# Kernel tuning notes

Hardware: AMD Instinct MI355X
Metric: run time of the kernel (lower is better)

The kernel has to match this reference:

```python
import jax, jax.numpy as jnp
import numpy as np

N = 524288
H = 128

def _mlp(x, w1, b1, w2, b2, w3, b3):
    # torch nn.Linear: y = x @ W^T + b, weights stored (out,in)
    x = jax.nn.relu(x @ w1.T + b1)
    x = jax.nn.relu(x @ w2.T + b2)
    return x @ w3.T + b3

def _det2(F):
    return F[:, 0, 0] * F[:, 1, 1] - F[:, 0, 1] * F[:, 1, 0]

def setup_inputs() -> dict:
    key = jax.random.key(0)
    ks = jax.random.split(key, 13)
    def lin(k, out_d, in_d):
        s = 1.0 / np.sqrt(in_d)
        kw, kb = jax.random.split(k)
        return (jax.random.uniform(kw, (out_d, in_d), jnp.float32, -s, s),
                jax.random.uniform(kb, (out_d,), jnp.float32, -s, s))
    F = jax.random.normal(ks[0], (N, 2, 2), jnp.float32)
    dc_w1, dc_b1 = lin(ks[1], H, 7)
    dc_w2, dc_b2 = lin(ks[2], H, H)
    dc_w3, dc_b3 = lin(ks[3], 4, H)
    sp_w1, sp_b1 = lin(ks[4], H, 3)
    sp_w2, sp_b2 = lin(ks[5], H, H)
    sp_w3, sp_b3 = lin(ks[6], 4, H)
    return dict(F=F, dc_w1=dc_w1, dc_b1=dc_b1, dc_w2=dc_w2, dc_b2=dc_b2,
                dc_w3=dc_w3, dc_b3=dc_b3, sp_w1=sp_w1, sp_b1=sp_b1,
                sp_w2=sp_w2, sp_b2=sp_b2, sp_w3=sp_w3, sp_b3=sp_b3)

def reference(F, dc_w1, dc_b1, dc_w2, dc_b2, dc_w3, dc_b3,
              sp_w1, sp_b1, sp_w2, sp_b2, sp_w3, sp_b3):
    I = jnp.eye(2, dtype=F.dtype)
    F = F.reshape(-1, 2, 2)
    # --- DeformationCorrector ---
    U, sig, Vh = jnp.linalg.svd(F)
    R = U @ Vh
    FtF = jnp.einsum('nji,njk->nik', F, F)  # F^T F
    I1 = sig - 1.0                           # (N,2)
    I2 = (FtF - I).reshape(-1, 4)            # (N,4)
    I3 = _det2(F)[:, None] - 1.0             # (N,1)
    inv = jnp.concatenate([I1, I2, I3], axis=1)  # (N,7)
    x = _mlp(inv, dc_w1, dc_b1, dc_w2, dc_b2, dc_w3, dc_b3).reshape(-1, 2, 2)
    x = (x + jnp.swapaxes(x, 1, 2)) * 0.5
    Fp = R @ x + F
    # --- StressPredictorFromFp ---
    U2, sig2, Vh2 = jnp.linalg.svd(Fp)
    R2 = U2 @ Vh2
    J1 = sig2.sum(axis=1) - 2.0
    J2 = jnp.sum(Fp * Fp, axis=(1, 2)) - 1.0  # trace(Fp^T Fp) - 1
    J3 = _det2(Fp) - 1.0
    y = jnp.stack([J1, J2, J3], axis=1)       # (N,3)
    y = _mlp(y, sp_w1, sp_b1, sp_w2, sp_b2, sp_w3, sp_b3).reshape(-1, 2, 2)
    y = (y + jnp.swapaxes(y, 1, 2)) * 0.5
    P = R2 @ y
    cauchy = jnp.einsum('nij,nkj->nik', P, Fp)  # P @ Fp^T
    return cauchy.reshape(-1, 4)
```

## Files before the change

### kernel.cpp

```cpp
#include <hip/hip_runtime.h>

typedef float f32x4 __attribute__((ext_vector_type(4)));
typedef _Float16 f16x8 __attribute__((ext_vector_type(8)));

#define OFF_W2H 0
#define OFF_W2L 32768
#define OFF_W1  65536
#define OFF_W3H 73728
#define OFF_W3L 75008
#define OFF_B1  76288
#define OFF_B2  76800
#define OFF_B3  77312
#define LDS_BYTES 77328

__device__ inline float kdet(float a, float b, float c, float d) {
    float w = b * c;
    float e = fmaf(b, c, -w);
    return fmaf(a, d, -w) - e;
}

__device__ inline void polar2(float a, float b, float c, float d, float det,
                              float& R00, float& R01, float& R10, float& R11) {
    if (det >= 0.f) {
        float h1 = a + d, h2 = c - b;
        float q = fmaxf(sqrtf(h1 * h1 + h2 * h2), 1e-30f);
        float iq = 1.f / q;
        R00 = h1 * iq; R01 = -h2 * iq; R10 = h2 * iq; R11 = h1 * iq;
    } else {
        float h1 = a - d, h2 = b + c;
        float q = fmaxf(sqrtf(h1 * h1 + h2 * h2), 1e-30f);
        float iq = 1.f / q;
        R00 = h1 * iq; R01 = h2 * iq; R10 = h2 * iq; R11 = -h1 * iq;
    }
}

__device__ inline void stage_weights(unsigned char* s, const float* w1, int D,
                                     const float* b1, const float* w2, const float* b2,
                                     const float* w3, const float* b3) {
    const int tid = threadIdx.x, nt = blockDim.x;
    for (int idx = tid; idx < 2048; idx += nt) {
        int j = idx >> 4, kb = (idx >> 2) & 3, g = idx & 3;
        const float* src = w2 + j * 128 + kb * 32 + g * 4;
        f16x8 vh, vl;
        #pragma unroll
        for (int e = 0; e < 8; ++e) {
            float w = src[(e & 3) + 16 * (e >> 2)];
            _Float16 h = (_Float16)w;
            vh[e] = h;
            vl[e] = (_Float16)(w - (float)h);
        }
        int off = j * 256 + ((kb * 64 + g * 16) ^ ((j & 7) << 4));
        *(f16x8*)(s + OFF_W2H + off) = vh;
        *(f16x8*)(s + OFF_W2L + off) = vl;
    }
    for (int idx = tid; idx < 512; idx += nt) {
        int j = idx >> 2, g = idx & 3;
        f16x8 v;
        #pragma unroll
        for (int e = 0; e < 8; ++e) {
            int k = 4 * g + (e & 3) + 16 * (e >> 2);
            _Float16 val = (_Float16)0.f;
            if (k < D) val = (_Float16)w1[j * D + k];
            else if (k >= 8 && k < 8 + D) val = (_Float16)w1[j * D + (k - 8)];
            else if (k >= 16 && k < 16 + D) {
                float w = w1[j * D + (k - 16)];
                val = (_Float16)(w - (float)(_Float16)w);
            }
            v[e] = val;
        }
        int gg = g ^ ((j ^ (j >> 2)) & 3);
        *(f16x8*)(s + OFF_W1 + j * 64 + gg * 16) = v;
    }
    for (int idx = tid; idx < 80; idx += nt) {
        int j = idx >> 4, kb = (idx >> 2) & 3, g = idx & 3;
        f16x8 vh, vl;
        #pragma unroll
        for (int e = 0; e < 8; ++e) {
            int c = 32 * kb + 4 * g + (e & 3) + 16 * (e >> 2);
            float w = (j < 4) ? w3[j * 128 + c] : 0.f;
            _Float16 h = (_Float16)w;
            vh[e] = h;
            vl[e] = (_Float16)(w - (float)h);
        }
        int off = j * 256 + ((kb * 64 + g * 16) ^ ((j & 7) << 4));
        *(f16x8*)(s + OFF_W3H + off) = vh;
        *(f16x8*)(s + OFF_W3L + off) = vl;
    }
    for (int idx = tid; idx < 128; idx += nt) {
        ((float*)(s + OFF_B1))[idx] = b1[idx];
        ((float*)(s + OFF_B2))[idx] = b2[idx];
    }
    if (tid < 4) ((float*)(s + OFF_B3))[tid] = b3[tid];
}

__device__ inline f16x8 build_b1(const float* xin, int g) {
    _Float16 xh[8], xl[8];
    #pragma unroll
    for (int c = 0; c < 8; ++c) {
        float v = xin[c];
        _Float16 h = (_Float16)v;
        xh[c] = h;
        xl[c] = (_Float16)(v - (float)h);
    }
    const _Float16 z = (_Float16)0.f;
    f16x8 b;
    if (g == 0) {
        b[0] = xh[0]; b[1] = xh[1]; b[2] = xh[2]; b[3] = xh[3];
        b[4] = xh[0]; b[5] = xh[1]; b[6] = xh[2]; b[7] = xh[3];
    } else if (g == 1) {
        b[0] = xh[4]; b[1] = xh[5]; b[2] = xh[6]; b[3] = xh[7];
        b[4] = xh[4]; b[5] = xh[5]; b[6] = xh[6]; b[7] = xh[7];
    } else if (g == 2) {
        b[0] = xl[0]; b[1] = xl[1]; b[2] = xl[2]; b[3] = xl[3];
        b[4] = z; b[5] = z; b[6] = z; b[7] = z;
    } else {
        b[0] = xl[4]; b[1] = xl[5]; b[2] = xl[6]; b[3] = xl[7];
        b[4] = z; b[5] = z; b[6] = z; b[7] = z;
    }
    return b;
}

__device__ inline void mlp128(const unsigned char* s, f16x8 b1f, int m, int g,
                              float xout[4]) {
    const f32x4 zero = {0.f, 0.f, 0.f, 0.f};
    f32x4 acc[8];
    #pragma unroll
    for (int mb = 0; mb < 8; ++mb) {
        int row = m + 16 * mb;
        int gg = g ^ ((row ^ (row >> 2)) & 3);
        f16x8 af = *(const f16x8*)(s + OFF_W1 + row * 64 + gg * 16);
        acc[mb] = __builtin_amdgcn_mfma_f32_16x16x32_f16(af, b1f, zero, 0, 0, 0);
    }
    #pragma unroll
    for (int mb = 0; mb < 8; ++mb) {
        f32x4 bq = *(const f32x4*)(s + OFF_B1 + (mb * 16 + g * 4) * 4);
        #pragma unroll
        for (int r = 0; r < 4; ++r) acc[mb][r] = fmaxf(acc[mb][r] + bq[r], 0.f);
    }
    f16x8 hh[4], hl[4];
    #pragma unroll
    for (int kb = 0; kb < 4; ++kb)
        #pragma unroll
        for (int e = 0; e < 8; ++e) {
            float v = acc[2 * kb + (e >> 2)][e & 3];
            _Float16 h = (_Float16)v;
            hh[kb][e] = h;
            hl[kb][e] = (_Float16)(v - (float)h);
        }
    f32x4 acc2[8];
    #pragma unroll
    for (int mb = 0; mb < 8; ++mb) acc2[mb] = zero;
    #pragma unroll
    for (int mb = 0; mb < 8; ++mb) {
        int row = m + 16 * mb;
        #pragma unroll
        for (int kb = 0; kb < 4; ++kb) {
            int off = row * 256 + ((kb * 64 + g * 16) ^ ((row & 7) << 4));
            f16x8 ah = *(const f16x8*)(s + OFF_W2H + off);
            f16x8 al = *(const f16x8*)(s + OFF_W2L + off);
            acc2[mb] = __builtin_amdgcn_mfma_f32_16x16x32_f16(ah, hh[kb], acc2[mb], 0, 0, 0);
            acc2[mb] = __builtin_amdgcn_mfma_f32_16x16x32_f16(ah, hl[kb], acc2[mb], 0, 0, 0);
            acc2[mb] = __builtin_amdgcn_mfma_f32_16x16x32_f16(al, hh[kb], acc2[mb], 0, 0, 0);
        }
    }
    #pragma unroll
    for (int mb = 0; mb < 8; ++mb) {
        f32x4 bq = *(const f32x4*)(s + OFF_B2 + (mb * 16 + g * 4) * 4);
        #pragma unroll
        for (int r = 0; r < 4; ++r) acc2[mb][r] = fmaxf(acc2[mb][r] + bq[r], 0.f);
    }
    f16x8 h2h[4], h2l[4];
    #pragma unroll
    for (int kb = 0; kb < 4; ++kb)
        #pragma unroll
        for (int e = 0; e < 8; ++e) {
            float v = acc2[2 * kb + (e >> 2)][e & 3];
            _Float16 h = (_Float16)v;
            h2h[kb][e] = h;
            h2l[kb][e] = (_Float16)(v - (float)h);
        }
    f32x4 acc3 = zero;
    const int r3 = (m < 4) ? m : 4;
    #pragma unroll
    for (int kb = 0; kb < 4; ++kb) {
        int off = r3 * 256 + ((kb * 64 + g * 16) ^ ((r3 & 7) << 4));
        f16x8 ah = *(const f16x8*)(s + OFF_W3H + off);
        f16x8 al = *(const f16x8*)(s + OFF_W3L + off);
        acc3 = __builtin_amdgcn_mfma_f32_16x16x32_f16(ah, h2h[kb], acc3, 0, 0, 0);
        acc3 = __builtin_amdgcn_mfma_f32_16x16x32_f16(ah, h2l[kb], acc3, 0, 0, 0);
        acc3 = __builtin_amdgcn_mfma_f32_16x16x32_f16(al, h2h[kb], acc3, 0, 0, 0);
    }
    f32x4 b3q = *(const f32x4*)(s + OFF_B3);
    #pragma unroll
    for (int o = 0; o < 4; ++o)
        xout[o] = __shfl(acc3[o] + b3q[o], m, 64);
}

__global__ __launch_bounds__(512) void k_dc(const float* __restrict__ Fin,
    const float* __restrict__ w1, const float* __restrict__ b1,
    const float* __restrict__ w2, const float* __restrict__ b2,
    const float* __restrict__ w3, const float* __restrict__ b3,
    float* __restrict__ out, int nelem) {
    extern __shared__ unsigned char s[];
    stage_weights(s, w1, 7, b1, w2, b2, w3, b3);
    __syncthreads();
    const int lane = threadIdx.x & 63;
    const int m = lane & 15, g = lane >> 4;
    const int wid = blockIdx.x * (blockDim.x >> 6) + (threadIdx.x >> 6);
    const int nw = gridDim.x * (blockDim.x >> 6);
    const int niter = nelem >> 4;
    for (int it = wid; it < niter; it += nw) {
        const int elem = it * 16 + m;
        f32x4 f = ((const f32x4*)Fin)[elem];
        float a = f[0], b = f[1], c = f[2], d = f[3];
        float det = kdet(a, b, c, d);
        float R00, R01, R10, R11;
        polar2(a, b, c, d, det, R00, R01, R10, R11);
        float E = 0.5f * (a + d), Hh = 0.5f * (c - b);
        float Fv = 0.5f * (a - d), G = 0.5f * (b + c);
        float Q = sqrtf(E * E + Hh * Hh), Rr = sqrtf(Fv * Fv + G * G);
        float inv[8];
        inv[0] = Q + Rr - 1.f;
        inv[1] = fabsf(Q - Rr) - 1.f;
        inv[2] = fmaf(a, a, c * c) - 1.f;
        inv[3] = fmaf(a, b, c * d);
        inv[4] = inv[3];
        inv[5] = fmaf(b, b, d * d) - 1.f;
        inv[6] = det - 1.f;
        inv[7] = 0.f;
        f16x8 b1f = build_b1(inv, g);
        float x[4];
        mlp128(s, b1f, m, g, x);
        float x01 = 0.5f * (x[1] + x[2]);
        float Fp00 = fmaf(R00, x[0], fmaf(R01, x01, a));
        float Fp01 = fmaf(R00, x01, fmaf(R01, x[3], b));
        float Fp10 = fmaf(R10, x[0], fmaf(R11, x01, c));
        float Fp11 = fmaf(R10, x01, fmaf(R11, x[3], d));
        if (g == 0) {
            f32x4 r = {Fp00, Fp01, Fp10, Fp11};
            ((f32x4*)out)[elem] = r;
        }
    }
}

__global__ __launch_bounds__(512) void k_sp(float* io,
    const float* __restrict__ w1, const float* __restrict__ b1,
    const float* __restrict__ w2, const float* __restrict__ b2,
    const float* __restrict__ w3, const float* __restrict__ b3, int nelem) {
    extern __shared__ unsigned char s[];
    stage_weights(s, w1, 3, b1, w2, b2, w3, b3);
    __syncthreads();
    const int lane = threadIdx.x & 63;
    const int m = lane & 15, g = lane >> 4;
    const int wid = blockIdx.x * (blockDim.x >> 6) + (threadIdx.x >> 6);
    const int nw = gridDim.x * (blockDim.x >> 6);
    const int niter = nelem >> 4;
    for (int it = wid; it < niter; it += nw) {
        const int elem = it * 16 + m;
        f32x4 fp = ((const f32x4*)io)[elem];
        float a = fp[0], b = fp[1], c = fp[2], d = fp[3];
        float det = kdet(a, b, c, d);
        float R00, R01, R10, R11;
        polar2(a, b, c, d, det, R00, R01, R10, R11);
        float E = 0.5f * (a + d), Hh = 0.5f * (c - b);
        float Fv = 0.5f * (a - d), G = 0.5f * (b + c);
        float Q = sqrtf(E * E + Hh * Hh), Rr = sqrtf(Fv * Fv + G * G);
        float inv[8];
        inv[0] = (Q + Rr) + fabsf(Q - Rr) - 2.f;
        inv[1] = fmaf(a, a, fmaf(b, b, fmaf(c, c, d * d))) - 1.f;
        inv[2] = det - 1.f;
        inv[3] = 0.f; inv[4] = 0.f; inv[5] = 0.f; inv[6] = 0.f; inv[7] = 0.f;
        f16x8 b1f = build_b1(inv, g);
        float y[4];
        mlp128(s, b1f, m, g, y);
        float y01 = 0.5f * (y[1] + y[2]);
        float P00 = fmaf(R00, y[0], R01 * y01);
        float P01 = fmaf(R00, y01, R01 * y[3]);
        float P10 = fmaf(R10, y[0], R11 * y01);
        float P11 = fmaf(R10, y01, R11 * y[3]);
        float C00 = fmaf(P00, a, P01 * b);
        float C01 = fmaf(P00, c, P01 * d);
        float C10 = fmaf(P10, a, P11 * b);
        float C11 = fmaf(P10, c, P11 * d);
        if (g == 0) {
            f32x4 r = {C00, C01, C10, C11};
            ((f32x4*)io)[elem] = r;
        }
    }
}

extern "C" void kernel_launch(void* const* d_in, const int* in_sizes, int n_in,
                              void* d_out, int out_size, void* d_ws, size_t ws_size,
                              hipStream_t stream) {
    const float* F     = (const float*)d_in[0];
    const float* dc_w1 = (const float*)d_in[1];
    const float* dc_b1 = (const float*)d_in[2];
    const float* dc_w2 = (const float*)d_in[3];
    const float* dc_b2 = (const float*)d_in[4];
    const float* dc_w3 = (const float*)d_in[5];
    const float* dc_b3 = (const float*)d_in[6];
    const float* sp_w1 = (const float*)d_in[7];
    const float* sp_b1 = (const float*)d_in[8];
    const float* sp_w2 = (const float*)d_in[9];
    const float* sp_b2 = (const float*)d_in[10];
    const float* sp_w3 = (const float*)d_in[11];
    const float* sp_b3 = (const float*)d_in[12];
    float* out = (float*)d_out;
    const int nelem = in_sizes[0] / 4;
    hipFuncSetAttribute((const void*)k_dc,
                        hipFuncAttributeMaxDynamicSharedMemorySize, LDS_BYTES);
    hipFuncSetAttribute((const void*)k_sp,
                        hipFuncAttributeMaxDynamicSharedMemorySize, LDS_BYTES);
    dim3 grid(512), block(512);
    k_dc<<<grid, block, LDS_BYTES, stream>>>(F, dc_w1, dc_b1, dc_w2, dc_b2,
                                             dc_w3, dc_b3, out, nelem);
    k_sp<<<grid, block, LDS_BYTES, stream>>>(out, sp_w1, sp_b1, sp_w2, sp_b2,
                                             sp_w3, sp_b3, nelem);
}
```

Baseline: 127.5 us.

## Process two 16-element tiles per wave to reuse LDS weight fragments

Each wave now handles 32 elements per iteration by running two independent MLP pipelines (A and B) that share every weight fragment loaded from LDS. This halves LDS weight reads per element and gives the MFMA unit two independent dependency chains to interleave. Block size drops to 256 threads with launch_bounds(256,2), and build_b1 is rewritten with selects instead of branches. The cost is roughly double the accumulator and fragment registers per thread, which may cause spills or lower occupancy; with LDS at about 77KB per block, fewer waves per CU may be resident.

```diff
diff --git a/kernel.cpp b/kernel.cpp
--- a/kernel.cpp
+++ b/kernel.cpp
@@ -12,6 +12,8 @@
 #define OFF_B2  76800
 #define OFF_B3  77312
 #define LDS_BYTES 77328
+
+#define MFMA16(A, B, C) __builtin_amdgcn_mfma_f32_16x16x32_f16(A, B, C, 0, 0, 0)
 
 __device__ inline float kdet(float a, float b, float c, float d) {
     float w = b * c;
@@ -93,63 +95,64 @@
     if (tid < 4) ((float*)(s + OFF_B3))[tid] = b3[tid];
 }
 
-__device__ inline f16x8 build_b1(const float* xin, int g) {
-    _Float16 xh[8], xl[8];
-    #pragma unroll
-    for (int c = 0; c < 8; ++c) {
-        float v = xin[c];
-        _Float16 h = (_Float16)v;
-        xh[c] = h;
-        xl[c] = (_Float16)(v - (float)h);
-    }
+__device__ inline f16x8 build_b1(const float in[8], int g) {
+    const bool half2 = (g & 1);
+    float t0 = half2 ? in[4] : in[0];
+    float t1 = half2 ? in[5] : in[1];
+    float t2 = half2 ? in[6] : in[2];
+    float t3 = half2 ? in[7] : in[3];
+    _Float16 h0 = (_Float16)t0, h1 = (_Float16)t1;
+    _Float16 h2 = (_Float16)t2, h3 = (_Float16)t3;
+    _Float16 l0 = (_Float16)(t0 - (float)h0), l1 = (_Float16)(t1 - (float)h1);
+    _Float16 l2 = (_Float16)(t2 - (float)h2), l3 = (_Float16)(t3 - (float)h3);
+    const bool hi = (g < 2);
     const _Float16 z = (_Float16)0.f;
     f16x8 b;
-    if (g == 0) {
-        b[0] = xh[0]; b[1] = xh[1]; b[2] = xh[2]; b[3] = xh[3];
-        b[4] = xh[0]; b[5] = xh[1]; b[6] = xh[2]; b[7] = xh[3];
-    } else if (g == 1) {
-        b[0] = xh[4]; b[1] = xh[5]; b[2] = xh[6]; b[3] = xh[7];
-        b[4] = xh[4]; b[5] = xh[5]; b[6] = xh[6]; b[7] = xh[7];
-    } else if (g == 2) {
-        b[0] = xl[0]; b[1] = xl[1]; b[2] = xl[2]; b[3] = xl[3];
-        b[4] = z; b[5] = z; b[6] = z; b[7] = z;
-    } else {
-        b[0] = xl[4]; b[1] = xl[5]; b[2] = xl[6]; b[3] = xl[7];
-        b[4] = z; b[5] = z; b[6] = z; b[7] = z;
-    }
+    b[0] = hi ? h0 : l0; b[1] = hi ? h1 : l1;
+    b[2] = hi ? h2 : l2; b[3] = hi ? h3 : l3;
+    b[4] = hi ? h0 : z;  b[5] = hi ? h1 : z;
+    b[6] = hi ? h2 : z;  b[7] = hi ? h3 : z;
     return b;
 }
 
-__device__ inline void mlp128(const unsigned char* s, f16x8 b1f, int m, int g,
-                              float xout[4]) {
+__device__ inline void mlp128x2(const unsigned char* s, f16x8 b1fA, f16x8 b1fB,
+                                int m, int g, float xA[4], float xB[4]) {
     const f32x4 zero = {0.f, 0.f, 0.f, 0.f};
-    f32x4 acc[8];
+    f32x4 accA[8], accB[8];
     #pragma unroll
     for (int mb = 0; mb < 8; ++mb) {
         int row = m + 16 * mb;
         int gg = g ^ ((row ^ (row >> 2)) & 3);
         f16x8 af = *(const f16x8*)(s + OFF_W1 + row * 64 + gg * 16);
-        acc[mb] = __builtin_amdgcn_mfma_f32_16x16x32_f16(af, b1f, zero, 0, 0, 0);
+        accA[mb] = MFMA16(af, b1fA, zero);
+        accB[mb] = MFMA16(af, b1fB, zero);
     }
     #pragma unroll
     for (int mb = 0; mb < 8; ++mb) {
         f32x4 bq = *(const f32x4*)(s + OFF_B1 + (mb * 16 + g * 4) * 4);
         #pragma unroll
-        for (int r = 0; r < 4; ++r) acc[mb][r] = fmaxf(acc[mb][r] + bq[r], 0.f);
-    }
-    f16x8 hh[4], hl[4];
+        for (int r = 0; r < 4; ++r) {
+            accA[mb][r] = fmaxf(accA[mb][r] + bq[r], 0.f);
+            accB[mb][r] = fmaxf(accB[mb][r] + bq[r], 0.f);
+        }
+    }
+    f16x8 hhA[4], hlA[4], hhB[4], hlB[4];
     #pragma unroll
     for (int kb = 0; kb < 4; ++kb)
         #pragma unroll
         for (int e = 0; e < 8; ++e) {
-            float v = acc[2 * kb + (e >> 2)][e & 3];
-            _Float16 h = (_Float16)v;
-            hh[kb][e] = h;
-            hl[kb][e] = (_Float16)(v - (float)h);
-        }
-    f32x4 acc2[8];
-    #pragma unroll
-    for (int mb = 0; mb < 8; ++mb) acc2[mb] = zero;
+            float vA = accA[2 * kb + (e >> 2)][e & 3];
+            _Float16 hA = (_Float16)vA;
+            hhA[kb][e] = hA;
+            hlA[kb][e] = (_Float16)(vA - (float)hA);
+            float vB = accB[2 * kb + (e >> 2)][e & 3];
+            _Float16 hB = (_Float16)vB;
+            hhB[kb][e] = hB;
+            hlB[kb][e] = (_Float16)(vB - (float)hB);
+        }
+    f32x4 acc2A[8], acc2B[8];
+    #pragma unroll
+    for (int mb = 0; mb < 8; ++mb) { acc2A[mb] = zero; acc2B[mb] = zero; }
     #pragma unroll
     for (int mb = 0; mb < 8; ++mb) {
         int row = m + 16 * mb;
@@ -158,45 +161,122 @@
             int off = row * 256 + ((kb * 64 + g * 16) ^ ((row & 7) << 4));
             f16x8 ah = *(const f16x8*)(s + OFF_W2H + off);
             f16x8 al = *(const f16x8*)(s + OFF_W2L + off);
-            acc2[mb] = __builtin_amdgcn_mfma_f32_16x16x32_f16(ah, hh[kb], acc2[mb], 0, 0, 0);
-            acc2[mb] = __builtin_amdgcn_mfma_f32_16x16x32_f16(ah, hl[kb], acc2[mb], 0, 0, 0);
-            acc2[mb] = __builtin_amdgcn_mfma_f32_16x16x32_f16(al, hh[kb], acc2[mb], 0, 0, 0);
+            acc2A[mb] = MFMA16(ah, hhA[kb], acc2A[mb]);
+            acc2A[mb] = MFMA16(ah, hlA[kb], acc2A[mb]);
+            acc2A[mb] = MFMA16(al, hhA[kb], acc2A[mb]);
+            acc2B[mb] = MFMA16(ah, hhB[kb], acc2B[mb]);
+            acc2B[mb] = MFMA16(ah, hlB[kb], acc2B[mb]);
+            acc2B[mb] = MFMA16(al, hhB[kb], acc2B[mb]);
         }
     }
     #pragma unroll
     for (int mb = 0; mb < 8; ++mb) {
         f32x4 bq = *(const f32x4*)(s + OFF_B2 + (mb * 16 + g * 4) * 4);
         #pragma unroll
-        for (int r = 0; r < 4; ++r) acc2[mb][r] = fmaxf(acc2[mb][r] + bq[r], 0.f);
-    }
-    f16x8 h2h[4], h2l[4];
+        for (int r = 0; r < 4; ++r) {
+            acc2A[mb][r] = fmaxf(acc2A[mb][r] + bq[r], 0.f);
+            acc2B[mb][r] = fmaxf(acc2B[mb][r] + bq[r], 0.f);
+        }
+    }
+    f16x8 h2hA[4], h2lA[4], h2hB[4], h2lB[4];
     #pragma unroll
     for (int kb = 0; kb < 4; ++kb)
         #pragma unroll
         for (int e = 0; e < 8; ++e) {
-            float v = acc2[2 * kb + (e >> 2)][e & 3];
-            _Float16 h = (_Float16)v;
-            h2h[kb][e] = h;
-            h2l[kb][e] = (_Float16)(v - (float)h);
-        }
-    f32x4 acc3 = zero;
+            float vA = acc2A[2 * kb + (e >> 2)][e & 3];
+            _Float16 hA = (_Float16)vA;
+            h2hA[kb][e] = hA;
+            h2lA[kb][e] = (_Float16)(vA - (float)hA);
+            float vB = acc2B[2 * kb + (e >> 2)][e & 3];
+            _Float16 hB = (_Float16)vB;
+            h2hB[kb][e] = hB;
+            h2lB[kb][e] = (_Float16)(vB - (float)hB);
+        }
+    f32x4 acc3A = zero, acc3B = zero;
     const int r3 = (m < 4) ? m : 4;
     #pragma unroll
     for (int kb = 0; kb < 4; ++kb) {
         int off = r3 * 256 + ((kb * 64 + g * 16) ^ ((r3 & 7) << 4));
         f16x8 ah = *(const f16x8*)(s + OFF_W3H + off);
         f16x8 al = *(const f16x8*)(s + OFF_W3L + off);
-        acc3 = __builtin_amdgcn_mfma_f32_16x16x32_f16(ah, h2h[kb], acc3, 0, 0, 0);
-        acc3 = __builtin_amdgcn_mfma_f32_16x16x32_f16(ah, h2l[kb], acc3, 0, 0, 0);
-        acc3 = __builtin_amdgcn_mfma_f32_16x16x32_f16(al, h2h[kb], acc3, 0, 0, 0);
+        acc3A = MFMA16(ah, h2hA[kb], acc3A);
+        acc3A = MFMA16(ah, h2lA[kb], acc3A);
+        acc3A = MFMA16(al, h2hA[kb], acc3A);
+        acc3B = MFMA16(ah, h2hB[kb], acc3B);
+        acc3B = MFMA16(ah, h2lB[kb], acc3B);
+        acc3B = MFMA16(al, h2hB[kb], acc3B);
     }
     f32x4 b3q = *(const f32x4*)(s + OFF_B3);
     #pragma unroll
-    for (int o = 0; o < 4; ++o)
-        xout[o] = __shfl(acc3[o] + b3q[o], m, 64);
-}
-
-__global__ __launch_bounds__(512) void k_dc(const float* __restrict__ Fin,
+    for (int o = 0; o < 4; ++o) {
+        xA[o] = __shfl(acc3A[o] + b3q[o], m, 64);
+        xB[o] = __shfl(acc3B[o] + b3q[o], m, 64);
+    }
+}
+
+__device__ inline f16x8 dc_pre(const f32x4 f, int g, float& R00, float& R01,
+                               float& R10, float& R11) {
+    float a = f[0], b = f[1], c = f[2], d = f[3];
+    float det = kdet(a, b, c, d);
+    polar2(a, b, c, d, det, R00, R01, R10, R11);
+    float E = 0.5f * (a + d), Hh = 0.5f * (c - b);
+    float Fv = 0.5f * (a - d), G = 0.5f * (b + c);
+    float Q = sqrtf(E * E + Hh * Hh), Rr = sqrtf(Fv * Fv + G * G);
+    float inv[8];
+    inv[0] = Q + Rr - 1.f;
+    inv[1] = fabsf(Q - Rr) - 1.f;
+    inv[2] = fmaf(a, a, c * c) - 1.f;
+    inv[3] = fmaf(a, b, c * d);
+    inv[4] = inv[3];
+    inv[5] = fmaf(b, b, d * d) - 1.f;
+    inv[6] = det - 1.f;
+    inv[7] = 0.f;
+    return build_b1(inv, g);
+}
+
+__device__ inline f16x8 sp_pre(const f32x4 fp, int g, float& R00, float& R01,
+                               float& R10, float& R11) {
+    float a = fp[0], b = fp[1], c = fp[2], d = fp[3];
+    float det = kdet(a, b, c, d);
+    polar2(a, b, c, d, det, R00, R01, R10, R11);
+    float E = 0.5f * (a + d), Hh = 0.5f * (c - b);
+    float Fv = 0.5f * (a - d), G = 0.5f * (b + c);
+    float Q = sqrtf(E * E + Hh * Hh), Rr = sqrtf(Fv * Fv + G * G);
+    float inv[8];
+    inv[0] = (Q + Rr) + fabsf(Q - Rr) - 2.f;
+    inv[1] = fmaf(a, a, fmaf(b, b, fmaf(c, c, d * d))) - 1.f;
+    inv[2] = det - 1.f;
+    inv[3] = 0.f; inv[4] = 0.f; inv[5] = 0.f; inv[6] = 0.f; inv[7] = 0.f;
+    return build_b1(inv, g);
+}
+
+__device__ inline f32x4 dc_post(const float x[4], const f32x4 f,
+                                float R00, float R01, float R10, float R11) {
+    float x01 = 0.5f * (x[1] + x[2]);
+    f32x4 r;
+    r[0] = fmaf(R00, x[0], fmaf(R01, x01, f[0]));
+    r[1] = fmaf(R00, x01, fmaf(R01, x[3], f[1]));
+    r[2] = fmaf(R10, x[0], fmaf(R11, x01, f[2]));
+    r[3] = fmaf(R10, x01, fmaf(R11, x[3], f[3]));
+    return r;
+}
+
+__device__ inline f32x4 sp_post(const float y[4], const f32x4 fp,
+                                float R00, float R01, float R10, float R11) {
+    float y01 = 0.5f * (y[1] + y[2]);
+    float P00 = fmaf(R00, y[0], R01 * y01);
+    float P01 = fmaf(R00, y01, R01 * y[3]);
+    float P10 = fmaf(R10, y[0], R11 * y01);
+    float P11 = fmaf(R10, y01, R11 * y[3]);
+    f32x4 r;
+    r[0] = fmaf(P00, fp[0], P01 * fp[1]);
+    r[1] = fmaf(P00, fp[2], P01 * fp[3]);
+    r[2] = fmaf(P10, fp[0], P11 * fp[1]);
+    r[3] = fmaf(P10, fp[2], P11 * fp[3]);
+    return r;
+}
+
+__global__ __launch_bounds__(256, 2) void k_dc(const float* __restrict__ Fin,
     const float* __restrict__ w1, const float* __restrict__ b1,
     const float* __restrict__ w2, const float* __restrict__ b2,
     const float* __restrict__ w3, const float* __restrict__ b3,
@@ -208,42 +288,26 @@
     const int m = lane & 15, g = lane >> 4;
     const int wid = blockIdx.x * (blockDim.x >> 6) + (threadIdx.x >> 6);
     const int nw = gridDim.x * (blockDim.x >> 6);
-    const int niter = nelem >> 4;
+    const int niter = nelem >> 5;
     for (int it = wid; it < niter; it += nw) {
-        const int elem = it * 16 + m;
-        f32x4 f = ((const f32x4*)Fin)[elem];
-        float a = f[0], b = f[1], c = f[2], d = f[3];
-        float det = kdet(a, b, c, d);
-        float R00, R01, R10, R11;
-        polar2(a, b, c, d, det, R00, R01, R10, R11);
-        float E = 0.5f * (a + d), Hh = 0.5f * (c - b);
-        float Fv = 0.5f * (a - d), G = 0.5f * (b + c);
-        float Q = sqrtf(E * E + Hh * Hh), Rr = sqrtf(Fv * Fv + G * G);
-        float inv[8];
-        inv[0] = Q + Rr - 1.f;
-        inv[1] = fabsf(Q - Rr) - 1.f;
-        inv[2] = fmaf(a, a, c * c) - 1.f;
-        inv[3] = fmaf(a, b, c * d);
-        inv[4] = inv[3];
-        inv[5] = fmaf(b, b, d * d) - 1.f;
-        inv[6] = det - 1.f;
-        inv[7] = 0.f;
-        f16x8 b1f = build_b1(inv, g);
-        float x[4];
-        mlp128(s, b1f, m, g, x);
-        float x01 = 0.5f * (x[1] + x[2]);
-        float Fp00 = fmaf(R00, x[0], fmaf(R01, x01, a));
-        float Fp01 = fmaf(R00, x01, fmaf(R01, x[3], b));
-        float Fp10 = fmaf(R10, x[0], fmaf(R11, x01, c));
-        float Fp11 = fmaf(R10, x01, fmaf(R11, x[3], d));
+        const int eA = it * 32 + m, eB = eA + 16;
+        f32x4 fA = ((const f32x4*)Fin)[eA];
+        f32x4 fB = ((const f32x4*)Fin)[eB];
+        float RA00, RA01, RA10, RA11, RB00, RB01, RB10, RB11;
+        f16x8 b1fA = dc_pre(fA, g, RA00, RA01, RA10, RA11);
+        f16x8 b1fB = dc_pre(fB, g, RB00, RB01, RB10, RB11);
+        float xA[4], xB[4];
+        mlp128x2(s, b1fA, b1fB, m, g, xA, xB);
+        f32x4 rA = dc_post(xA, fA, RA00, RA01, RA10, RA11);
+        f32x4 rB = dc_post(xB, fB, RB00, RB01, RB10, RB11);
         if (g == 0) {
-            f32x4 r = {Fp00, Fp01, Fp10, Fp11};
-            ((f32x4*)out)[elem] = r;
-        }
-    }
-}
-
-__global__ __launch_bounds__(512) void k_sp(float* io,
+            ((f32x4*)out)[eA] = rA;
+            ((f32x4*)out)[eB] = rB;
+        }
+    }
+}
+
+__global__ __launch_bounds__(256, 2) void k_sp(float* io,
     const float* __restrict__ w1, const float* __restrict__ b1,
     const float* __restrict__ w2, const float* __restrict__ b2,
     const float* __restrict__ w3, const float* __restrict__ b3, int nelem) {
@@ -254,37 +318,21 @@
     const int m = lane & 15, g = lane >> 4;
     const int wid = blockIdx.x * (blockDim.x >> 6) + (threadIdx.x >> 6);
     const int nw = gridDim.x * (blockDim.x >> 6);
-    const int niter = nelem >> 4;
+    const int niter = nelem >> 5;
     for (int it = wid; it < niter; it += nw) {
-        const int elem = it * 16 + m;
-        f32x4 fp = ((const f32x4*)io)[elem];
-        float a = fp[0], b = fp[1], c = fp[2], d = fp[3];
-        float det = kdet(a, b, c, d);
-        float R00, R01, R10, R11;
-        polar2(a, b, c, d, det, R00, R01, R10, R11);
-        float E = 0.5f * (a + d), Hh = 0.5f * (c - b);
-        float Fv = 0.5f * (a - d), G = 0.5f * (b + c);
-        float Q = sqrtf(E * E + Hh * Hh), Rr = sqrtf(Fv * Fv + G * G);
-        float inv[8];
-        inv[0] = (Q + Rr) + fabsf(Q - Rr) - 2.f;
-        inv[1] = fmaf(a, a, fmaf(b, b, fmaf(c, c, d * d))) - 1.f;
-        inv[2] = det - 1.f;
-        inv[3] = 0.f; inv[4] = 0.f; inv[5] = 0.f; inv[6] = 0.f; inv[7] = 0.f;
-        f16x8 b1f = build_b1(inv, g);
-        float y[4];
-        mlp128(s, b1f, m, g, y);
-        float y01 = 0.5f * (y[1] + y[2]);
-        float P00 = fmaf(R00, y[0], R01 * y01);
-        float P01 = fmaf(R00, y01, R01 * y[3]);
-        float P10 = fmaf(R10, y[0], R11 * y01);
-        float P11 = fmaf(R10, y01, R11 * y[3]);
-        float C00 = fmaf(P00, a, P01 * b);
-        float C01 = fmaf(P00, c, P01 * d);
-        float C10 = fmaf(P10, a, P11 * b);
-        float C11 = fmaf(P10, c, P11 * d);
+        const int eA = it * 32 + m, eB = eA + 16;
+        f32x4 fA = ((const f32x4*)io)[eA];
+        f32x4 fB = ((const f32x4*)io)[eB];
+        float RA00, RA01, RA10, RA11, RB00, RB01, RB10, RB11;
+        f16x8 b1fA = sp_pre(fA, g, RA00, RA01, RA10, RA11);
+        f16x8 b1fB = sp_pre(fB, g, RB00, RB01, RB10, RB11);
+        float yA[4], yB[4];
+        mlp128x2(s, b1fA, b1fB, m, g, yA, yB);
+        f32x4 rA = sp_post(yA, fA, RA00, RA01, RA10, RA11);
+        f32x4 rB = sp_post(yB, fB, RB00, RB01, RB10, RB11);
         if (g == 0) {
-            f32x4 r = {C00, C01, C10, C11};
-            ((f32x4*)io)[elem] = r;
+            ((f32x4*)io)[eA] = rA;
+            ((f32x4*)io)[eB] = rB;
         }
     }
 }
@@ -311,7 +359,7 @@
                         hipFuncAttributeMaxDynamicSharedMemorySize, LDS_BYTES);
     hipFuncSetAttribute((const void*)k_sp,
                         hipFuncAttributeMaxDynamicSharedMemorySize, LDS_BYTES);
-    dim3 grid(512), block(512);
+    dim3 grid(512), block(256);
     k_dc<<<grid, block, LDS_BYTES, stream>>>(F, dc_w1, dc_b1, dc_w2, dc_b2,
                                              dc_w3, dc_b3, out, nelem);
     k_sp<<<grid, block, LDS_BYTES, stream>>>(out, sp_w1, sp_b1, sp_w2, sp_b2,
```

Result: slower. 446.2 us (+250.0%).
